# Performance work log

Hardware: AMD Instinct MI355X
Metric: run time of the kernel (lower is better)

## Reference

```python
import jax, jax.numpy as jnp
import numpy as np

N = 50000      # nodes
E = 800000     # edges (avg degree 16)
D = 128        # hidden_channels
FFN = 512
BOT = 64
L = 3          # number of stacked GCN layers


def setup_inputs() -> dict:
    key = jax.random.key(0)
    ks = jax.random.split(key, 10)
    x = jax.random.normal(ks[0], (N, D), dtype=jnp.float32)
    edge_index = jax.random.randint(ks[1], (2, E), 0, N, dtype=jnp.int64)
    s = np.float32(1.0 / np.sqrt(D))
    conv_W = jax.random.normal(ks[2], (L, D, D), dtype=jnp.float32) * s
    conv_b = jnp.zeros((L, D), dtype=jnp.float32)
    fc1_w = jax.random.normal(ks[3], (D, FFN), dtype=jnp.float32) * s
    fc1_b = jnp.zeros((FFN,), dtype=jnp.float32)
    fc2_w = jax.random.normal(ks[4], (FFN, BOT), dtype=jnp.float32) * np.float32(1.0 / np.sqrt(FFN))
    fc2_b = jnp.zeros((BOT,), dtype=jnp.float32)
    return {"x": x, "edge_index": edge_index, "conv_W": conv_W, "conv_b": conv_b,
            "fc1_w": fc1_w, "fc1_b": fc1_b, "fc2_w": fc2_w, "fc2_b": fc2_b}


def _gcn_conv(x, src, dst, W, b):
    """GCNConv: D^{-1/2} (A+I) D^{-1/2} X W + b, degree computed with self-loops."""
    n = x.shape[0]
    deg = jax.ops.segment_sum(jnp.ones(src.shape[0], x.dtype), dst, num_segments=n) + 1.0
    norm = jax.lax.rsqrt(deg)                      # [N]
    xw = x @ W                                     # [N, D] transform before scatter
    coef = (norm[src] * norm[dst])[:, None]        # [E, 1]
    agg = jax.ops.segment_sum(xw[src] * coef, dst, num_segments=n)  # gather-scale-scatter
    return agg + xw * (norm * norm)[:, None] + b   # self-loop term + bias


def reference(x, edge_index, conv_W, conv_b, fc1_w, fc1_b, fc2_w, fc2_b):
    src, dst = edge_index[0], edge_index[1]
    for l in range(L):
        x = jax.nn.relu(_gcn_conv(x, src, dst, conv_W[l], conv_b[l]))
        # dropout = identity in eval mode
    x = jax.nn.relu(x @ fc1_w + fc1_b)
    return x @ fc2_w + fc2_b
```

## Files before the change

kernel.cpp:

```cpp
#include <hip/hip_runtime.h>
#include <hip/hip_fp16.h>

#define D 128
#define FFN 512
#define BOT 64
#define EPB 4096

typedef _Float16 f16x8 __attribute__((ext_vector_type(8)));
typedef float f32x4 __attribute__((ext_vector_type(4)));


__global__ __launch_bounds__(256) void k_bcnt(const int* __restrict__ dst, int* __restrict__ bcnt, int nE) {
  __shared__ int h[256];
  int t = threadIdx.x;
  h[t] = 0;
  __syncthreads();
  int base = blockIdx.x * EPB;
  #pragma unroll
  for (int m = 0; m < EPB / 256; ++m) {
    int idx = base + m * 256 + t;
    if (idx < nE) atomicAdd(&h[dst[idx] >> 8], 1);
  }
  __syncthreads();
  if (h[t] > 0) atomicAdd(&bcnt[t], h[t]);
}

__global__ __launch_bounds__(256) void k_bscan(const int* __restrict__ bcnt, int* __restrict__ boff,
                                               int* __restrict__ bcur, int nbkt, int nE) {
  __shared__ int s[256];
  int t = threadIdx.x;
  int v = (t < nbkt) ? bcnt[t] : 0;
  s[t] = v;
  __syncthreads();
  for (int d = 1; d < 256; d <<= 1) {
    int add = (t >= d) ? s[t - d] : 0;
    __syncthreads();
    s[t] += add;
    __syncthreads();
  }
  int ex = s[t] - v;
  boff[t] = ex;
  bcur[t] = ex;
  if (t == 255) boff[256] = nE;
  if (t >= nbkt) boff[t] = nE;
}

__global__ __launch_bounds__(256) void k_bscatter(const int* __restrict__ ei, int* __restrict__ bcur,
                                                  uint2* __restrict__ bed, int nE) {
  __shared__ uint2 st[EPB];
  __shared__ int cnt[256], off[256], base[256], cur[256];
  int t = threadIdx.x;
  int blk0 = blockIdx.x * EPB;
  int nblk = nE - blk0;
  if (nblk > EPB) nblk = EPB;

  cnt[t] = 0;
  cur[t] = 0;
  __syncthreads();

  int rs[EPB / 256], rd[EPB / 256];
  #pragma unroll
  for (int m = 0; m < EPB / 256; ++m) {
    int idx = blk0 + m * 256 + t;
    if (idx < nE) {
      rs[m] = ei[idx];
      rd[m] = ei[nE + idx];
      atomicAdd(&cnt[rd[m] >> 8], 1);
    } else {
      rd[m] = -1;
    }
  }
  __syncthreads();

  int v = cnt[t];
  off[t] = v;
  __syncthreads();
  for (int d = 1; d < 256; d <<= 1) {
    int add = (t >= d) ? off[t - d] : 0;
    __syncthreads();
    off[t] += add;
    __syncthreads();
  }
  int ex = off[t] - v;
  __syncthreads();
  off[t] = ex;
  base[t] = (v > 0) ? atomicAdd(&bcur[t], v) : 0;
  __syncthreads();

  #pragma unroll
  for (int m = 0; m < EPB / 256; ++m) {
    if (rd[m] >= 0) {
      int b = rd[m] >> 8;
      int p = off[b] + atomicAdd(&cur[b], 1);
      st[p] = make_uint2((unsigned)rs[m], (unsigned)rd[m]);
    }
  }
  __syncthreads();

  for (int j = t; j < nblk; j += 256) {
    uint2 pr = st[j];
    int b = (int)(pr.y >> 8);
    bed[base[b] + (j - off[b])] = pr;
  }
}

__global__ __launch_bounds__(256) void k_bcsr(const uint2* __restrict__ bed, const int* __restrict__ boff,
                                              int* __restrict__ rowptr, float* __restrict__ nrm,
                                              int* __restrict__ col, int N, int nE) {
  __shared__ int cnt[256], noff[256], cur[256];
  int t = threadIdx.x;
  int b = blockIdx.x;
  int e0 = boff[b], e1 = boff[b + 1];

  cnt[t] = 0;
  __syncthreads();
  for (int j = e0 + t; j < e1; j += 256)
    atomicAdd(&cnt[bed[j].y & 255], 1);
  __syncthreads();

  int v = cnt[t];
  noff[t] = v;
  __syncthreads();
  for (int d = 1; d < 256; d <<= 1) {
    int add = (t >= d) ? noff[t - d] : 0;
    __syncthreads();
    noff[t] += add;
    __syncthreads();
  }
  int ex = noff[t] - v;
  __syncthreads();
  noff[t] = ex;
  cur[t] = ex;
  __syncthreads();

  int node = (b << 8) + t;
  if (node < N) {
    rowptr[node] = e0 + ex;
    nrm[node] = rsqrtf((float)v + 1.0f);
  }
  if (b == 0 && t == 0) rowptr[N] = nE;

  for (int j = e0 + t; j < e1; j += 256) {
    uint2 pr = bed[j];
    int d2 = (int)(pr.y & 255);
    int p = atomicAdd(&cur[d2], 1);
    col[e0 + p] = (int)pr.x;
  }
}


__global__ __launch_bounds__(256) void k_split(const float* __restrict__ X,
                                               __half* __restrict__ Xh, __half* __restrict__ Xl, int n8) {
  int i = blockIdx.x * 256 + threadIdx.x;
  if (i >= n8) return;
  float4 a = ((const float4*)X)[i * 2];
  float4 b = ((const float4*)X)[i * 2 + 1];
  float v[8] = {a.x, a.y, a.z, a.w, b.x, b.y, b.z, b.w};
  __half2 hh[4], ll[4];
  #pragma unroll
  for (int q = 0; q < 4; ++q) {
    __half h0 = __float2half_rn(v[2 * q]);
    __half h1 = __float2half_rn(v[2 * q + 1]);
    __half l0 = __float2half_rn(v[2 * q] - __half2float(h0));
    __half l1 = __float2half_rn(v[2 * q + 1] - __half2float(h1));
    hh[q] = __halves2half2(h0, h1);
    ll[q] = __halves2half2(l0, l1);
  }
  *(uint4*)(Xh + (size_t)i * 8) = *(uint4*)hh;
  *(uint4*)(Xl + (size_t)i * 8) = *(uint4*)ll;
}

__global__ __launch_bounds__(256) void k_splitw(const float* __restrict__ W,
                                                __half* __restrict__ WhT, __half* __restrict__ WlT,
                                                int K, int N) {
  int id = blockIdx.x * 256 + threadIdx.x;
  if (id >= K * N) return;
  int n = id / K, k = id % K;
  float v = W[(size_t)k * N + n];
  __half h = __float2half_rn(v);
  WhT[id] = h;
  WlT[id] = __float2half_rn(v - __half2float(h));
}

__global__ __launch_bounds__(256) void k_splitwc(const float* __restrict__ W,
                                                 __half* __restrict__ WhT, __half* __restrict__ WlT,
                                                 int total) {
  int id = blockIdx.x * 256 + threadIdx.x;
  if (id >= total) return;
  int l = id / (D * D), r = id % (D * D);
  int n = r / D, k = r % D;
  float v = W[(size_t)l * D * D + (size_t)k * D + n];
  __half h = __float2half_rn(v);
  WhT[id] = h;
  WlT[id] = __float2half_rn(v - __half2float(h));
}


template<int BN, int MODE, int NSPLIT>
__global__ __launch_bounds__(256, (BN == 128) ? 3 : 4)
void k_mfma(const __half* __restrict__ Ah_g, const __half* __restrict__ Al_g,
            const __half* __restrict__ BhT_g, const __half* __restrict__ BlT_g,
            const float* __restrict__ aux, void* __restrict__ Cout,
            int M, int K, int ldc, int nRB) {
  constexpr int NR = BN / 32;
  constexpr int ALR = (NSPLIT == 2) ? 128 : 1;
  __shared__ __half Ahs[128][40];
  __shared__ __half Als[ALR][40];
  __shared__ __half Bhs[BN][40];
  __shared__ __half Bls[BN][40];

  const int t = threadIdx.x;
  const int rb = blockIdx.x % nRB, cb = blockIdx.x / nRB;
  const int rbase = rb * 128, cbase = cb * BN;
  const int lane = t & 63, wid = t >> 6;
  const int wr = (wid >> 1) * 64;
  const int wc = (wid & 1) * (BN / 2);
  const int lr = lane & 15, lq = lane >> 4;

  f32x4 acc[4][NR];
  #pragma unroll
  for (int m = 0; m < 4; ++m)
    #pragma unroll
    for (int n = 0; n < NR; ++n) acc[m][n] = (f32x4){0.f, 0.f, 0.f, 0.f};

  for (int kc = 0; kc < K; kc += 32) {
    __syncthreads();
    #pragma unroll
    for (int mm = 0; mm < 2; ++mm) {
      int idx = mm * 256 + t;
      int row = idx >> 2, q = idx & 3;
      int gr = rbase + row;
      uint4 vh = {0, 0, 0, 0};
      if (gr < M) vh = *(const uint4*)(Ah_g + (size_t)gr * K + kc + q * 8);
      *(uint4*)&Ahs[row][q * 8] = vh;
      if constexpr (NSPLIT == 2) {
        uint4 vl = {0, 0, 0, 0};
        if (gr < M) vl = *(const uint4*)(Al_g + (size_t)gr * K + kc + q * 8);
        *(uint4*)&Als[row][q * 8] = vl;
      }
    }
    #pragma unroll
    for (int mm = 0; mm < BN / 64; ++mm) {
      int idx = mm * 256 + t;
      int c = idx >> 2, q = idx & 3;
      size_t src = (size_t)(cbase + c) * K + kc + q * 8;
      *(uint4*)&Bhs[c][q * 8] = *(const uint4*)(BhT_g + src);
      *(uint4*)&Bls[c][q * 8] = *(const uint4*)(BlT_g + src);
    }
    __syncthreads();

    f16x8 fb[NR], fbl[NR], fa[4];
    #pragma unroll
    for (int n = 0; n < NR; ++n) {
      fb[n]  = *(const f16x8*)&Bhs[wc + n * 16 + lr][lq * 8];
      fbl[n] = *(const f16x8*)&Bls[wc + n * 16 + lr][lq * 8];
    }
    #pragma unroll
    for (int m = 0; m < 4; ++m)
      fa[m] = *(const f16x8*)&Ahs[wr + m * 16 + lr][lq * 8];

    #pragma unroll
    for (int m = 0; m < 4; ++m)
      #pragma unroll
      for (int n = 0; n < NR; ++n) {
        acc[m][n] = __builtin_amdgcn_mfma_f32_16x16x32_f16(fa[m], fb[n], acc[m][n], 0, 0, 0);
        acc[m][n] = __builtin_amdgcn_mfma_f32_16x16x32_f16(fa[m], fbl[n], acc[m][n], 0, 0, 0);
      }

    if constexpr (NSPLIT == 2) {
      f16x8 fal[4];
      #pragma unroll
      for (int m = 0; m < 4; ++m)
        fal[m] = *(const f16x8*)&Als[wr + m * 16 + lr][lq * 8];
      #pragma unroll
      for (int m = 0; m < 4; ++m)
        #pragma unroll
        for (int n = 0; n < NR; ++n)
          acc[m][n] = __builtin_amdgcn_mfma_f32_16x16x32_f16(fal[m], fb[n], acc[m][n], 0, 0, 0);
    }
  }

  if constexpr (MODE == 0) {
    __half* Yo = (__half*)Cout;
    #pragma unroll
    for (int m = 0; m < 4; ++m)
      #pragma unroll
      for (int j = 0; j < 4; ++j) {
        int row = rbase + wr + m * 16 + lq * 4 + j;
        if (row < M) {
          float s = aux[row];
          #pragma unroll
          for (int n = 0; n < NR; ++n) {
            int colg = cbase + wc + n * 16 + lr;
            Yo[(size_t)row * ldc + colg] = __float2half_rn(acc[m][n][j] * s);
          }
        }
      }
  } else {
    float bb[NR];
    #pragma unroll
    for (int n = 0; n < NR; ++n) bb[n] = aux[cbase + wc + n * 16 + lr];
    if constexpr (MODE == 1) {
      __half* Yo = (__half*)Cout;
      #pragma unroll
      for (int m = 0; m < 4; ++m)
        #pragma unroll
        for (int j = 0; j < 4; ++j) {
          int row = rbase + wr + m * 16 + lq * 4 + j;
          if (row < M) {
            #pragma unroll
            for (int n = 0; n < NR; ++n) {
              int colg = cbase + wc + n * 16 + lr;
              Yo[(size_t)row * ldc + colg] = __float2half_rn(fmaxf(acc[m][n][j] + bb[n], 0.f));
            }
          }
        }
    } else {
      float* Of = (float*)Cout;
      #pragma unroll
      for (int m = 0; m < 4; ++m)
        #pragma unroll
        for (int j = 0; j < 4; ++j) {
          int row = rbase + wr + m * 16 + lq * 4 + j;
          if (row < M) {
            #pragma unroll
            for (int n = 0; n < NR; ++n) {
              int colg = cbase + wc + n * 16 + lr;
              Of[(size_t)row * ldc + colg] = acc[m][n][j] + bb[n];
            }
          }
        }
    }
  }
}


__global__ __launch_bounds__(256) void k_agg(const __half* __restrict__ Y,
                                             const int* __restrict__ rowptr, const int* __restrict__ col,
                                             const float* __restrict__ nrm, const float* __restrict__ bias,
                                             __half2* __restrict__ Xh2, __half2* __restrict__ Xl2, int n) {
  int wid = (blockIdx.x * 256 + threadIdx.x) >> 6;
  int lane = threadIdx.x & 63;
  if (wid >= n) return;
  const __half2* Yv = (const __half2*)Y;
  float2 s0 = __half22float2(Yv[(size_t)wid * 64 + lane]);
  float2 s1 = make_float2(0.f, 0.f);
  float2 s2 = make_float2(0.f, 0.f);
  float2 s3 = make_float2(0.f, 0.f);
  int e0 = rowptr[wid], e1 = rowptr[wid + 1];
  int e = e0;
  for (; e + 4 <= e1; e += 4) {
    int c0 = col[e], c1 = col[e + 1], c2 = col[e + 2], c3 = col[e + 3];
    float2 v0 = __half22float2(Yv[(size_t)c0 * 64 + lane]);
    float2 v1 = __half22float2(Yv[(size_t)c1 * 64 + lane]);
    float2 v2 = __half22float2(Yv[(size_t)c2 * 64 + lane]);
    float2 v3 = __half22float2(Yv[(size_t)c3 * 64 + lane]);
    s0.x += v0.x; s0.y += v0.y;
    s1.x += v1.x; s1.y += v1.y;
    s2.x += v2.x; s2.y += v2.y;
    s3.x += v3.x; s3.y += v3.y;
  }
  for (; e < e1; ++e) {
    int c = col[e];
    float2 v = __half22float2(Yv[(size_t)c * 64 + lane]);
    s0.x += v.x; s0.y += v.y;
  }
  float2 s;
  s.x = (s0.x + s1.x) + (s2.x + s3.x);
  s.y = (s0.y + s1.y) + (s2.y + s3.y);
  float nm = nrm[wid];
  float2 bb = ((const float2*)bias)[lane];
  float ox = fmaxf(fmaf(s.x, nm, bb.x), 0.f);
  float oy = fmaxf(fmaf(s.y, nm, bb.y), 0.f);
  __half hx = __float2half_rn(ox), hy = __float2half_rn(oy);
  __half lx = __float2half_rn(ox - __half2float(hx));
  __half ly = __float2half_rn(oy - __half2float(hy));
  size_t idx = (size_t)wid * 64 + lane;
  Xh2[idx] = __halves2half2(hx, hy);
  Xl2[idx] = __halves2half2(lx, ly);
}

extern "C" void kernel_launch(void* const* d_in, const int* in_sizes, int n_in,
                              void* d_out, int out_size, void* d_ws, size_t ws_size,
                              hipStream_t stream) {
  const float* x     = (const float*)d_in[0];
  const int*   ei    = (const int*)d_in[1];
  const float* convW = (const float*)d_in[2];
  const float* convB = (const float*)d_in[3];
  const float* w1    = (const float*)d_in[4];
  const float* b1    = (const float*)d_in[5];
  const float* w2    = (const float*)d_in[6];
  const float* b2    = (const float*)d_in[7];
  float* out = (float*)d_out;

  int N = in_sizes[0] / D;
  int E = in_sizes[1] / 2;
  int L = in_sizes[2] / (D * D);
  int NBKT = (N + 255) >> 8;

  char* ws = (char*)d_ws;
  size_t off = 0;
  auto alloc = [&](size_t bytes) -> char* {
    char* p = ws + off;
    off += (bytes + 255) & ~(size_t)255;
    return p;
  };
  float*  nrm    = (float*)alloc((size_t)N * 4);
  int*    rowptr = (int*)alloc((size_t)(N + 1) * 4);
  int*    col    = (int*)alloc((size_t)E * 4);
  int*    bcnt   = (int*)alloc(512 * 4);
  int*    boff   = (int*)alloc(512 * 4);
  int*    bcur   = (int*)alloc(512 * 4);
  uint2*  bed    = (uint2*)alloc((size_t)E * 8);
  __half* Xh     = (__half*)alloc((size_t)N * D * 2);
  __half* Xl     = (__half*)alloc((size_t)N * D * 2);
  __half* Yh     = (__half*)alloc((size_t)N * D * 2);
  __half* Hh     = (__half*)alloc((size_t)N * FFN * 2);
  __half* WcTh   = (__half*)alloc((size_t)L * D * D * 2);
  __half* WcTl   = (__half*)alloc((size_t)L * D * D * 2);
  __half* W1Th   = (__half*)alloc((size_t)D * FFN * 2);
  __half* W1Tl   = (__half*)alloc((size_t)D * FFN * 2);
  __half* W2Th   = (__half*)alloc((size_t)FFN * BOT * 2);
  __half* W2Tl   = (__half*)alloc((size_t)FFN * BOT * 2);

  int gS = (E + EPB - 1) / EPB;
  hipMemsetAsync(bcnt, 0, 512 * 4, stream);
  k_bcnt<<<gS, 256, 0, stream>>>(ei + E, bcnt, E);
  k_bscan<<<1, 256, 0, stream>>>(bcnt, boff, bcur, NBKT, E);
  k_bscatter<<<gS, 256, 0, stream>>>(ei, bcur, bed, E);
  k_bcsr<<<NBKT, 256, 0, stream>>>(bed, boff, rowptr, nrm, col, N, E);

  int n8 = N * D / 8;
  k_split<<<(n8 + 255) / 256, 256, 0, stream>>>(x, Xh, Xl, n8);
  k_splitwc<<<(L * D * D + 255) / 256, 256, 0, stream>>>(convW, WcTh, WcTl, L * D * D);
  k_splitw<<<(D * FFN + 255) / 256, 256, 0, stream>>>(w1, W1Th, W1Tl, D, FFN);
  k_splitw<<<(FFN * BOT + 255) / 256, 256, 0, stream>>>(w2, W2Th, W2Tl, FFN, BOT);

  int nRB = (N + 127) / 128;
  for (int l = 0; l < L; ++l) {
    k_mfma<128, 0, 2><<<nRB, 256, 0, stream>>>(
        Xh, Xl, WcTh + (size_t)l * D * D, WcTl + (size_t)l * D * D, nrm, Yh, N, D, D, nRB);
    k_agg<<<(N + 3) / 4, 256, 0, stream>>>(Yh, rowptr, col, nrm, convB + (size_t)l * D,
                                           (__half2*)Xh, (__half2*)Xl, N);
  }

  k_mfma<128, 1, 2><<<nRB * (FFN / 128), 256, 0, stream>>>(
      Xh, Xl, W1Th, W1Tl, b1, Hh, N, D, FFN, nRB);
  k_mfma<64, 2, 1><<<nRB, 256, 0, stream>>>(
      Hh, (const __half*)nullptr, W2Th, W2Tl, b2, out, N, FFN, BOT, nRB);
}
```

Baseline: 282.3 us.

## Fuse FFN layers into one MLP kernel and retile conv GEMM and aggregation

Replaces the two FFN GEMM launches with a single fused kernel that computes each 64-column chunk of the hidden layer in shared memory, applies bias and ReLU, and accumulates straight into the output. This removes the N×512 fp16 intermediate write and re-read. The conv GEMM moves to 64-row tiles with higher occupancy. The aggregation kernel now uses 32 lanes per node with 8-byte loads, so each wave processes two nodes. The trade-off is that the fused MLP reloads the X tiles for each of the 8 FFN chunks and synchronizes more often.

```diff
diff --git a/kernel.cpp b/kernel.cpp
--- a/kernel.cpp
+++ b/kernel.cpp
@@ -196,188 +196,288 @@
 }
 
 
-template<int BN, int MODE, int NSPLIT>
-__global__ __launch_bounds__(256, (BN == 128) ? 3 : 4)
-void k_mfma(const __half* __restrict__ Ah_g, const __half* __restrict__ Al_g,
+__global__ __launch_bounds__(256, 4)
+void k_conv(const __half* __restrict__ Ah_g, const __half* __restrict__ Al_g,
             const __half* __restrict__ BhT_g, const __half* __restrict__ BlT_g,
-            const float* __restrict__ aux, void* __restrict__ Cout,
-            int M, int K, int ldc, int nRB) {
-  constexpr int NR = BN / 32;
-  constexpr int ALR = (NSPLIT == 2) ? 128 : 1;
-  __shared__ __half Ahs[128][40];
-  __shared__ __half Als[ALR][40];
-  __shared__ __half Bhs[BN][40];
-  __shared__ __half Bls[BN][40];
+            const float* __restrict__ aux, __half* __restrict__ Yo, int M) {
+  __shared__ __half Ahs[64][40];
+  __shared__ __half Als[64][40];
+  __shared__ __half Bhs[128][40];
+  __shared__ __half Bls[128][40];
 
   const int t = threadIdx.x;
-  const int rb = blockIdx.x % nRB, cb = blockIdx.x / nRB;
-  const int rbase = rb * 128, cbase = cb * BN;
+  const int rbase = blockIdx.x * 64;
   const int lane = t & 63, wid = t >> 6;
-  const int wr = (wid >> 1) * 64;
-  const int wc = (wid & 1) * (BN / 2);
+  const int wr = (wid >> 1) * 32;
+  const int wc = (wid & 1) * 64;
   const int lr = lane & 15, lq = lane >> 4;
 
-  f32x4 acc[4][NR];
-  #pragma unroll
-  for (int m = 0; m < 4; ++m)
-    #pragma unroll
-    for (int n = 0; n < NR; ++n) acc[m][n] = (f32x4){0.f, 0.f, 0.f, 0.f};
-
-  for (int kc = 0; kc < K; kc += 32) {
-    __syncthreads();
+  f32x4 acc[2][4];
+  #pragma unroll
+  for (int m = 0; m < 2; ++m)
+    #pragma unroll
+    for (int n = 0; n < 4; ++n) acc[m][n] = (f32x4){0.f, 0.f, 0.f, 0.f};
+
+  for (int kc = 0; kc < D; kc += 32) {
+    __syncthreads();
+    {
+      int row = t >> 2, q = t & 3;
+      int gr = rbase + row;
+      uint4 vh = {0, 0, 0, 0}, vl = {0, 0, 0, 0};
+      if (gr < M) {
+        vh = *(const uint4*)(Ah_g + (size_t)gr * D + kc + q * 8);
+        vl = *(const uint4*)(Al_g + (size_t)gr * D + kc + q * 8);
+      }
+      *(uint4*)&Ahs[row][q * 8] = vh;
+      *(uint4*)&Als[row][q * 8] = vl;
+    }
     #pragma unroll
     for (int mm = 0; mm < 2; ++mm) {
       int idx = mm * 256 + t;
-      int row = idx >> 2, q = idx & 3;
-      int gr = rbase + row;
-      uint4 vh = {0, 0, 0, 0};
-      if (gr < M) vh = *(const uint4*)(Ah_g + (size_t)gr * K + kc + q * 8);
-      *(uint4*)&Ahs[row][q * 8] = vh;
-      if constexpr (NSPLIT == 2) {
-        uint4 vl = {0, 0, 0, 0};
-        if (gr < M) vl = *(const uint4*)(Al_g + (size_t)gr * K + kc + q * 8);
-        *(uint4*)&Als[row][q * 8] = vl;
-      }
-    }
-    #pragma unroll
-    for (int mm = 0; mm < BN / 64; ++mm) {
-      int idx = mm * 256 + t;
       int c = idx >> 2, q = idx & 3;
-      size_t src = (size_t)(cbase + c) * K + kc + q * 8;
+      size_t src = (size_t)c * D + kc + q * 8;
       *(uint4*)&Bhs[c][q * 8] = *(const uint4*)(BhT_g + src);
       *(uint4*)&Bls[c][q * 8] = *(const uint4*)(BlT_g + src);
     }
     __syncthreads();
 
-    f16x8 fb[NR], fbl[NR], fa[4];
-    #pragma unroll
-    for (int n = 0; n < NR; ++n) {
+    f16x8 fa[2], fal[2], fb[4], fbl[4];
+    #pragma unroll
+    for (int m = 0; m < 2; ++m) {
+      fa[m]  = *(const f16x8*)&Ahs[wr + m * 16 + lr][lq * 8];
+      fal[m] = *(const f16x8*)&Als[wr + m * 16 + lr][lq * 8];
+    }
+    #pragma unroll
+    for (int n = 0; n < 4; ++n) {
       fb[n]  = *(const f16x8*)&Bhs[wc + n * 16 + lr][lq * 8];
       fbl[n] = *(const f16x8*)&Bls[wc + n * 16 + lr][lq * 8];
     }
     #pragma unroll
-    for (int m = 0; m < 4; ++m)
-      fa[m] = *(const f16x8*)&Ahs[wr + m * 16 + lr][lq * 8];
-
-    #pragma unroll
-    for (int m = 0; m < 4; ++m)
-      #pragma unroll
-      for (int n = 0; n < NR; ++n) {
+    for (int m = 0; m < 2; ++m)
+      #pragma unroll
+      for (int n = 0; n < 4; ++n) {
         acc[m][n] = __builtin_amdgcn_mfma_f32_16x16x32_f16(fa[m], fb[n], acc[m][n], 0, 0, 0);
         acc[m][n] = __builtin_amdgcn_mfma_f32_16x16x32_f16(fa[m], fbl[n], acc[m][n], 0, 0, 0);
-      }
-
-    if constexpr (NSPLIT == 2) {
-      f16x8 fal[4];
-      #pragma unroll
-      for (int m = 0; m < 4; ++m)
-        fal[m] = *(const f16x8*)&Als[wr + m * 16 + lr][lq * 8];
-      #pragma unroll
-      for (int m = 0; m < 4; ++m)
+        acc[m][n] = __builtin_amdgcn_mfma_f32_16x16x32_f16(fal[m], fb[n], acc[m][n], 0, 0, 0);
+      }
+  }
+
+  #pragma unroll
+  for (int m = 0; m < 2; ++m)
+    #pragma unroll
+    for (int j = 0; j < 4; ++j) {
+      int row = rbase + wr + m * 16 + lq * 4 + j;
+      if (row < M) {
+        float s = aux[row];
         #pragma unroll
-        for (int n = 0; n < NR; ++n)
-          acc[m][n] = __builtin_amdgcn_mfma_f32_16x16x32_f16(fal[m], fb[n], acc[m][n], 0, 0, 0);
-    }
-  }
-
-  if constexpr (MODE == 0) {
-    __half* Yo = (__half*)Cout;
-    #pragma unroll
-    for (int m = 0; m < 4; ++m)
-      #pragma unroll
-      for (int j = 0; j < 4; ++j) {
-        int row = rbase + wr + m * 16 + lq * 4 + j;
-        if (row < M) {
-          float s = aux[row];
+        for (int n = 0; n < 4; ++n) {
+          int colg = wc + n * 16 + lr;
+          Yo[(size_t)row * D + colg] = __float2half_rn(acc[m][n][j] * s);
+        }
+      }
+    }
+}
+
+
+__global__ __launch_bounds__(256, 3)
+void k_mlp(const __half* __restrict__ Xh_g, const __half* __restrict__ Xl_g,
+           const __half* __restrict__ W1hT, const __half* __restrict__ W1lT,
+           const float* __restrict__ B1,
+           const __half* __restrict__ W2hT, const __half* __restrict__ W2lT,
+           const float* __restrict__ B2,
+           float* __restrict__ Out, int M) {
+  __shared__ __half Xhs[64][40], Xls[64][40];
+  __shared__ __half W1hs[64][40], W1ls[64][40];
+  __shared__ __half Hs[2][64][40];
+  __shared__ __half W2hs[2][64][40], W2ls[2][64][40];
+
+  const int t = threadIdx.x;
+  const int rbase = blockIdx.x * 64;
+  const int lane = t & 63, wid = t >> 6;
+  const int wr = (wid >> 1) * 32;
+  const int wcn = (wid & 1) * 32;
+  const int lr = lane & 15, lq = lane >> 4;
+
+  f32x4 accO[2][2];
+  #pragma unroll
+  for (int m = 0; m < 2; ++m)
+    #pragma unroll
+    for (int n = 0; n < 2; ++n) accO[m][n] = (f32x4){0.f, 0.f, 0.f, 0.f};
+
+  for (int ch = 0; ch < FFN / 64; ++ch) {
+    f32x4 accH[2][2];
+    #pragma unroll
+    for (int m = 0; m < 2; ++m)
+      #pragma unroll
+      for (int n = 0; n < 2; ++n) accH[m][n] = (f32x4){0.f, 0.f, 0.f, 0.f};
+
+    for (int kc = 0; kc < D; kc += 32) {
+      __syncthreads();
+      {
+        int row = t >> 2, q = t & 3;
+        int gr = rbase + row;
+        uint4 vh = {0, 0, 0, 0}, vl = {0, 0, 0, 0};
+        if (gr < M) {
+          vh = *(const uint4*)(Xh_g + (size_t)gr * D + kc + q * 8);
+          vl = *(const uint4*)(Xl_g + (size_t)gr * D + kc + q * 8);
+        }
+        *(uint4*)&Xhs[row][q * 8] = vh;
+        *(uint4*)&Xls[row][q * 8] = vl;
+      }
+      {
+        int c = t >> 2, q = t & 3;
+        size_t src = (size_t)(ch * 64 + c) * D + kc + q * 8;
+        *(uint4*)&W1hs[c][q * 8] = *(const uint4*)(W1hT + src);
+        *(uint4*)&W1ls[c][q * 8] = *(const uint4*)(W1lT + src);
+      }
+      __syncthreads();
+
+      f16x8 fa[2], fal[2], fb[2], fbl[2];
+      #pragma unroll
+      for (int m = 0; m < 2; ++m) {
+        fa[m]  = *(const f16x8*)&Xhs[wr + m * 16 + lr][lq * 8];
+        fal[m] = *(const f16x8*)&Xls[wr + m * 16 + lr][lq * 8];
+      }
+      #pragma unroll
+      for (int n = 0; n < 2; ++n) {
+        fb[n]  = *(const f16x8*)&W1hs[wcn + n * 16 + lr][lq * 8];
+        fbl[n] = *(const f16x8*)&W1ls[wcn + n * 16 + lr][lq * 8];
+      }
+      #pragma unroll
+      for (int m = 0; m < 2; ++m)
+        #pragma unroll
+        for (int n = 0; n < 2; ++n) {
+          accH[m][n] = __builtin_amdgcn_mfma_f32_16x16x32_f16(fa[m], fb[n], accH[m][n], 0, 0, 0);
+          accH[m][n] = __builtin_amdgcn_mfma_f32_16x16x32_f16(fa[m], fbl[n], accH[m][n], 0, 0, 0);
+          accH[m][n] = __builtin_amdgcn_mfma_f32_16x16x32_f16(fal[m], fb[n], accH[m][n], 0, 0, 0);
+        }
+    }
+
+    __syncthreads();
+    {
+      float bb1[2];
+      #pragma unroll
+      for (int n = 0; n < 2; ++n) bb1[n] = B1[ch * 64 + wcn + n * 16 + lr];
+      #pragma unroll
+      for (int m = 0; m < 2; ++m)
+        #pragma unroll
+        for (int n = 0; n < 2; ++n)
           #pragma unroll
-          for (int n = 0; n < NR; ++n) {
-            int colg = cbase + wc + n * 16 + lr;
-            Yo[(size_t)row * ldc + colg] = __float2half_rn(acc[m][n][j] * s);
+          for (int j = 0; j < 4; ++j) {
+            int rl = wr + m * 16 + lq * 4 + j;
+            int cl = wcn + n * 16 + lr;
+            Hs[cl >> 5][rl][cl & 31] = __float2half_rn(fmaxf(accH[m][n][j] + bb1[n], 0.f));
           }
+    }
+    #pragma unroll
+    for (int s = 0; s < 2; ++s) {
+      int c = t >> 2, q = t & 3;
+      size_t src = (size_t)c * FFN + ch * 64 + s * 32 + q * 8;
+      *(uint4*)&W2hs[s][c][q * 8] = *(const uint4*)(W2hT + src);
+      *(uint4*)&W2ls[s][c][q * 8] = *(const uint4*)(W2lT + src);
+    }
+    __syncthreads();
+
+    #pragma unroll
+    for (int s = 0; s < 2; ++s) {
+      f16x8 fha[2], fwb[2], fwbl[2];
+      #pragma unroll
+      for (int m = 0; m < 2; ++m)
+        fha[m] = *(const f16x8*)&Hs[s][wr + m * 16 + lr][lq * 8];
+      #pragma unroll
+      for (int n = 0; n < 2; ++n) {
+        fwb[n]  = *(const f16x8*)&W2hs[s][wcn + n * 16 + lr][lq * 8];
+        fwbl[n] = *(const f16x8*)&W2ls[s][wcn + n * 16 + lr][lq * 8];
+      }
+      #pragma unroll
+      for (int m = 0; m < 2; ++m)
+        #pragma unroll
+        for (int n = 0; n < 2; ++n) {
+          accO[m][n] = __builtin_amdgcn_mfma_f32_16x16x32_f16(fha[m], fwb[n], accO[m][n], 0, 0, 0);
+          accO[m][n] = __builtin_amdgcn_mfma_f32_16x16x32_f16(fha[m], fwbl[n], accO[m][n], 0, 0, 0);
         }
-      }
-  } else {
-    float bb[NR];
-    #pragma unroll
-    for (int n = 0; n < NR; ++n) bb[n] = aux[cbase + wc + n * 16 + lr];
-    if constexpr (MODE == 1) {
-      __half* Yo = (__half*)Cout;
-      #pragma unroll
-      for (int m = 0; m < 4; ++m)
+    }
+  }
+
+  #pragma unroll
+  for (int m = 0; m < 2; ++m)
+    #pragma unroll
+    for (int j = 0; j < 4; ++j) {
+      int row = rbase + wr + m * 16 + lq * 4 + j;
+      if (row < M) {
         #pragma unroll
-        for (int j = 0; j < 4; ++j) {
-          int row = rbase + wr + m * 16 + lq * 4 + j;
-          if (row < M) {
-            #pragma unroll
-            for (int n = 0; n < NR; ++n) {
-              int colg = cbase + wc + n * 16 + lr;
-              Yo[(size_t)row * ldc + colg] = __float2half_rn(fmaxf(acc[m][n][j] + bb[n], 0.f));
-            }
-          }
+        for (int n = 0; n < 2; ++n) {
+          int colg = wcn + n * 16 + lr;
+          Out[(size_t)row * BOT + colg] = accO[m][n][j] + B2[colg];
         }
-    } else {
-      float* Of = (float*)Cout;
-      #pragma unroll
-      for (int m = 0; m < 4; ++m)
-        #pragma unroll
-        for (int j = 0; j < 4; ++j) {
-          int row = rbase + wr + m * 16 + lq * 4 + j;
-          if (row < M) {
-            #pragma unroll
-            for (int n = 0; n < NR; ++n) {
-              int colg = cbase + wc + n * 16 + lr;
-              Of[(size_t)row * ldc + colg] = acc[m][n][j] + bb[n];
-            }
-          }
-        }
-    }
-  }
+      }
+    }
 }
 
 
 __global__ __launch_bounds__(256) void k_agg(const __half* __restrict__ Y,
                                              const int* __restrict__ rowptr, const int* __restrict__ col,
                                              const float* __restrict__ nrm, const float* __restrict__ bias,
-                                             __half2* __restrict__ Xh2, __half2* __restrict__ Xl2, int n) {
-  int wid = (blockIdx.x * 256 + threadIdx.x) >> 6;
-  int lane = threadIdx.x & 63;
-  if (wid >= n) return;
-  const __half2* Yv = (const __half2*)Y;
-  float2 s0 = __half22float2(Yv[(size_t)wid * 64 + lane]);
-  float2 s1 = make_float2(0.f, 0.f);
-  float2 s2 = make_float2(0.f, 0.f);
-  float2 s3 = make_float2(0.f, 0.f);
-  int e0 = rowptr[wid], e1 = rowptr[wid + 1];
+                                             __half* __restrict__ Xh, __half* __restrict__ Xl, int n) {
+  int gtid = blockIdx.x * 256 + threadIdx.x;
+  int node = gtid >> 5;
+  int sl = threadIdx.x & 31;
+  if (node >= n) return;
+  const uint2* Yv = (const uint2*)Y;
+
+  auto up = [](uint2 v, float4& a) {
+    __half2 h0 = *(__half2*)&v.x, h1 = *(__half2*)&v.y;
+    float2 f0 = __half22float2(h0), f1 = __half22float2(h1);
+    a.x += f0.x; a.y += f0.y; a.z += f1.x; a.w += f1.y;
+  };
+
+  float4 s0 = {0.f, 0.f, 0.f, 0.f}, s1 = {0.f, 0.f, 0.f, 0.f};
+  float4 s2 = {0.f, 0.f, 0.f, 0.f}, s3 = {0.f, 0.f, 0.f, 0.f};
+  up(Yv[(size_t)node * 32 + sl], s0);
+  int e0 = rowptr[node], e1 = rowptr[node + 1];
   int e = e0;
   for (; e + 4 <= e1; e += 4) {
     int c0 = col[e], c1 = col[e + 1], c2 = col[e + 2], c3 = col[e + 3];
-    float2 v0 = __half22float2(Yv[(size_t)c0 * 64 + lane]);
-    float2 v1 = __half22float2(Yv[(size_t)c1 * 64 + lane]);
-    float2 v2 = __half22float2(Yv[(size_t)c2 * 64 + lane]);
-    float2 v3 = __half22float2(Yv[(size_t)c3 * 64 + lane]);
-    s0.x += v0.x; s0.y += v0.y;
-    s1.x += v1.x; s1.y += v1.y;
-    s2.x += v2.x; s2.y += v2.y;
-    s3.x += v3.x; s3.y += v3.y;
-  }
-  for (; e < e1; ++e) {
-    int c = col[e];
-    float2 v = __half22float2(Yv[(size_t)c * 64 + lane]);
-    s0.x += v.x; s0.y += v.y;
-  }
-  float2 s;
+    uint2 v0 = Yv[(size_t)c0 * 32 + sl];
+    uint2 v1 = Yv[(size_t)c1 * 32 + sl];
+    uint2 v2 = Yv[(size_t)c2 * 32 + sl];
+    uint2 v3 = Yv[(size_t)c3 * 32 + sl];
+    up(v0, s0); up(v1, s1); up(v2, s2); up(v3, s3);
+  }
+  for (; e < e1; ++e) up(Yv[(size_t)col[e] * 32 + sl], s0);
+
+  float4 s;
   s.x = (s0.x + s1.x) + (s2.x + s3.x);
   s.y = (s0.y + s1.y) + (s2.y + s3.y);
-  float nm = nrm[wid];
-  float2 bb = ((const float2*)bias)[lane];
-  float ox = fmaxf(fmaf(s.x, nm, bb.x), 0.f);
-  float oy = fmaxf(fmaf(s.y, nm, bb.y), 0.f);
-  __half hx = __float2half_rn(ox), hy = __float2half_rn(oy);
-  __half lx = __float2half_rn(ox - __half2float(hx));
-  __half ly = __float2half_rn(oy - __half2float(hy));
-  size_t idx = (size_t)wid * 64 + lane;
-  Xh2[idx] = __halves2half2(hx, hy);
-  Xl2[idx] = __halves2half2(lx, ly);
+  s.z = (s0.z + s1.z) + (s2.z + s3.z);
+  s.w = (s0.w + s1.w) + (s2.w + s3.w);
+
+  float nm = nrm[node];
+  float4 bb = ((const float4*)bias)[sl];
+  float o[4];
+  o[0] = fmaxf(fmaf(s.x, nm, bb.x), 0.f);
+  o[1] = fmaxf(fmaf(s.y, nm, bb.y), 0.f);
+  o[2] = fmaxf(fmaf(s.z, nm, bb.z), 0.f);
+  o[3] = fmaxf(fmaf(s.w, nm, bb.w), 0.f);
+
+  __half h[4], l[4];
+  #pragma unroll
+  for (int q = 0; q < 4; ++q) {
+    h[q] = __float2half_rn(o[q]);
+    l[q] = __float2half_rn(o[q] - __half2float(h[q]));
+  }
+  uint2 ph, pl;
+  ph.x = *(unsigned*)&(*(__half2*)&h[0]);
+  __half2 h23 = __halves2half2(h[2], h[3]);
+  ph.y = *(unsigned*)&h23;
+  __half2 l01 = __halves2half2(l[0], l[1]);
+  __half2 l23 = __halves2half2(l[2], l[3]);
+  pl.x = *(unsigned*)&l01;
+  pl.y = *(unsigned*)&l23;
+  __half2 h01 = __halves2half2(h[0], h[1]);
+  ph.x = *(unsigned*)&h01;
+  ((uint2*)Xh)[(size_t)node * 32 + sl] = ph;
+  ((uint2*)Xl)[(size_t)node * 32 + sl] = pl;
 }
 
 extern "C" void kernel_launch(void* const* d_in, const int* in_sizes, int n_in,
@@ -415,7 +515,6 @@
   __half* Xh     = (__half*)alloc((size_t)N * D * 2);
   __half* Xl     = (__half*)alloc((size_t)N * D * 2);
   __half* Yh     = (__half*)alloc((size_t)N * D * 2);
-  __half* Hh     = (__half*)alloc((size_t)N * FFN * 2);
   __half* WcTh   = (__half*)alloc((size_t)L * D * D * 2);
   __half* WcTl   = (__half*)alloc((size_t)L * D * D * 2);
   __half* W1Th   = (__half*)alloc((size_t)D * FFN * 2);
@@ -436,16 +535,13 @@
   k_splitw<<<(D * FFN + 255) / 256, 256, 0, stream>>>(w1, W1Th, W1Tl, D, FFN);
   k_splitw<<<(FFN * BOT + 255) / 256, 256, 0, stream>>>(w2, W2Th, W2Tl, FFN, BOT);
 
-  int nRB = (N + 127) / 128;
+  int nRB = (N + 63) / 64;
   for (int l = 0; l < L; ++l) {
-    k_mfma<128, 0, 2><<<nRB, 256, 0, stream>>>(
-        Xh, Xl, WcTh + (size_t)l * D * D, WcTl + (size_t)l * D * D, nrm, Yh, N, D, D, nRB);
-    k_agg<<<(N + 3) / 4, 256, 0, stream>>>(Yh, rowptr, col, nrm, convB + (size_t)l * D,
-                                           (__half2*)Xh, (__half2*)Xl, N);
-  }
-
-  k_mfma<128, 1, 2><<<nRB * (FFN / 128), 256, 0, stream>>>(
-      Xh, Xl, W1Th, W1Tl, b1, Hh, N, D, FFN, nRB);
-  k_mfma<64, 2, 1><<<nRB, 256, 0, stream>>>(
-      Hh, (const __half*)nullptr, W2Th, W2Tl, b2, out, N, FFN, BOT, nRB);
-}
+    k_conv<<<nRB, 256, 0, stream>>>(
+        Xh, Xl, WcTh + (size_t)l * D * D, WcTl + (size_t)l * D * D, nrm, Yh, N);
+    k_agg<<<(N * 32 + 255) / 256, 256, 0, stream>>>(Yh, rowptr, col, nrm, convB + (size_t)l * D,
+                                                    Xh, Xl, N);
+  }
+
+  k_mlp<<<nRB, 256, 0, stream>>>(Xh, Xl, W1Th, W1Tl, b1, W2Th, W2Tl, b2, out, N);
+}
```

Measured after the change: 271.0 us. 1.04x faster.
